# Optimization experiments

Measured on AMD Instinct MI355X. Metric: run time of the kernel, lower is better.

## Reference

```python
import jax, jax.numpy as jnp
import numpy as np

N, OUT, IN = 16384, 2048, 2048

def setup_inputs() -> dict:
    key = jax.random.key(0)
    k1, k2, k3 = jax.random.split(key, 3)
    input_ = jax.random.normal(k1, (N, IN), dtype=jnp.float32)
    # kaiming normal, fan_in mode: std = sqrt(2/fan_in)
    weight = jax.random.normal(k2, (OUT, IN), dtype=jnp.float32) * np.sqrt(2.0 / IN)
    mask = jax.random.randint(k3, (OUT, IN), 0, 2, dtype=jnp.int32)
    return {"input_": input_, "weight": weight, "mask": mask}

def reference(input_, weight, mask):
    # out = x @ (W * mask)^T  -- mask is a fixed binary expander pattern
    masked_w = weight * mask.astype(weight.dtype)  # [OUT, IN]
    return jnp.matmul(input_, masked_w.T)          # [N, OUT]
```

## Files before the change

kernel.cpp:

```cpp
#include <hip/hip_runtime.h>


#define MDIM 16384
#define NDIM 2048
#define KDIM 2048

#define BM 256
#define BN 256
#define NITER (KDIM / 128)
#define GRID_X ((MDIM / BM) * (NDIM / BN))

using f32x4   = __attribute__((ext_vector_type(4))) float;
using bf16x8  = __attribute__((ext_vector_type(8))) __bf16;
using ushort8 = __attribute__((ext_vector_type(8))) unsigned short;

__device__ __forceinline__ unsigned short f2bf(float f) {
  unsigned int u = __builtin_bit_cast(unsigned int, f);
  u = u + 0x7FFFu + ((u >> 16) & 1u);
  return (unsigned short)(u >> 16);
}


__global__ void convert_input_kernel(const float* __restrict__ in,
                                     unsigned short* __restrict__ out) {
  size_t base = ((size_t)blockIdx.x * blockDim.x + threadIdx.x) * 8;
  float4 a = *reinterpret_cast<const float4*>(in + base);
  float4 b = *reinterpret_cast<const float4*>(in + base + 4);
  ushort8 v;
  v[0] = f2bf(a.x); v[1] = f2bf(a.y); v[2] = f2bf(a.z); v[3] = f2bf(a.w);
  v[4] = f2bf(b.x); v[5] = f2bf(b.y); v[6] = f2bf(b.z); v[7] = f2bf(b.w);
  *reinterpret_cast<ushort8*>(out + base) = v;
}

__global__ void convert_weight_kernel(const float* __restrict__ w,
                                      const int* __restrict__ mk,
                                      unsigned short* __restrict__ out) {
  size_t base = ((size_t)blockIdx.x * blockDim.x + threadIdx.x) * 8;
  float4 a = *reinterpret_cast<const float4*>(w + base);
  float4 b = *reinterpret_cast<const float4*>(w + base + 4);
  int4 m0 = *reinterpret_cast<const int4*>(mk + base);
  int4 m1 = *reinterpret_cast<const int4*>(mk + base + 4);
  ushort8 v;
  v[0] = m0.x ? f2bf(a.x) : (unsigned short)0;
  v[1] = m0.y ? f2bf(a.y) : (unsigned short)0;
  v[2] = m0.z ? f2bf(a.z) : (unsigned short)0;
  v[3] = m0.w ? f2bf(a.w) : (unsigned short)0;
  v[4] = m1.x ? f2bf(b.x) : (unsigned short)0;
  v[5] = m1.y ? f2bf(b.y) : (unsigned short)0;
  v[6] = m1.z ? f2bf(b.z) : (unsigned short)0;
  v[7] = m1.w ? f2bf(b.w) : (unsigned short)0;
  *reinterpret_cast<ushort8*>(out + base) = v;
}


__device__ __forceinline__ f32x4 MF(bf16x8 a, bf16x8 b, f32x4 c) {
  return __builtin_amdgcn_mfma_f32_16x16x32_bf16(a, b, c, 0, 0, 0);
}
__device__ __forceinline__ void bar() {
  asm volatile("" ::: "memory");
  __builtin_amdgcn_s_barrier();
  asm volatile("" ::: "memory");
}
#define VMCNT(n) asm volatile("s_waitcnt vmcnt(" #n ")" ::: "memory")

__global__ __launch_bounds__(512, 2) void gemm4p(
    const unsigned short* __restrict__ Abf,
    const unsigned short* __restrict__ Bbf,
    float* __restrict__ C) {
  __shared__ __attribute__((aligned(16))) unsigned short Asl[4 * 8192];
  __shared__ __attribute__((aligned(16))) unsigned short Bsl[4 * 8192];

  int bid = blockIdx.x;
  int wgs = (bid & 7) * (GRID_X / 8) + (bid >> 3);
  int tm = wgs >> 3;
  int tn = wgs & 7;
  int row0 = tm * BM, col0 = tn * BN;

  int t = threadIdx.x;
  int lane = t & 63, wid = t >> 6;
  int wr = wid >> 2, wc = wid & 3;
  int fr = lane & 15, fq = lane >> 4;

  int p0 = (wid * 2 + 0) * 64 + lane;
  int p1 = (wid * 2 + 1) * 64 + lane;
  int r0 = p0 >> 2, kc0 = ((p0 & 3) ^ ((r0 >> 1) & 3)) * 8;
  int r1 = p1 >> 2, kc1 = ((p1 & 3) ^ ((r1 >> 1) & 3)) * 8;
  size_t offA0 = (size_t)(row0 + r0) * KDIM + kc0;
  size_t offA1 = (size_t)(row0 + r1) * KDIM + kc1;
  size_t offB0 = (size_t)(col0 + r0) * KDIM + kc0;
  size_t offB1 = (size_t)(col0 + r1) * KDIM + kc1;
  int ldsw0 = (wid * 2 + 0) * 512;
  int ldsw1 = (wid * 2 + 1) * 512;

  int kxor = (fq ^ ((fr >> 1) & 3)) * 8;
  int aoff = (wr * 128 + fr) * 32 + kxor;
  int boff = (wc * 64 + fr) * 32 + kxor;

  f32x4 acc[8][4];
#pragma unroll
  for (int m = 0; m < 8; ++m)
#pragma unroll
    for (int n = 0; n < 4; ++n) acc[m][n] = f32x4{0.f, 0.f, 0.f, 0.f};

#define SLOT_A(b, kh) (Asl + ((b) * 2 + (kh)) * 8192)
#define SLOT_B(b, kh) (Bsl + ((b) * 2 + (kh)) * 8192)

#define STG(slot, base, o0, o1, ke) do {                                        \
  __builtin_amdgcn_global_load_lds(                                             \
      (const __attribute__((address_space(1))) void*)((base) + (o0) + (ke)),    \
      (__attribute__((address_space(3))) void*)((slot) + ldsw0), 16, 0, 0);     \
  __builtin_amdgcn_global_load_lds(                                             \
      (const __attribute__((address_space(1))) void*)((base) + (o1) + (ke)),    \
      (__attribute__((address_space(3))) void*)((slot) + ldsw1), 16, 0, 0);     \
} while (0)

#define PHASE(b, kh, STAGES, WAITS) do {                                        \
  const unsigned short* _ap = SLOT_A(b, kh) + aoff;                             \
  const unsigned short* _bp = SLOT_B(b, kh) + boff;                             \
  bf16x8 _afr[8], _bfr[4];                                                      \
  _afr[0] = *(const bf16x8*)(_ap);                                              \
  _Pragma("unroll")                                                             \
  for (int _n = 0; _n < 4; ++_n) _bfr[_n] = *(const bf16x8*)(_bp + _n * 512);   \
  _Pragma("unroll")                                                             \
  for (int _m = 1; _m < 8; ++_m) _afr[_m] = *(const bf16x8*)(_ap + _m * 512);   \
  STAGES;                                                                       \
  WAITS;                                                                        \
  bar();                                                                        \
  __builtin_amdgcn_s_setprio(1);                                                \
  _Pragma("unroll")                                                             \
  for (int _m = 0; _m < 8; ++_m)                                                \
    _Pragma("unroll")                                                           \
    for (int _n = 0; _n < 4; ++_n)                                              \
      acc[_m][_n] = MF(_afr[_m], _bfr[_n], acc[_m][_n]);                        \
  __builtin_amdgcn_s_setprio(0);                                                \
  bar();                                                                        \
} while (0)

  STG(SLOT_A(0, 0), Abf, offA0, offA1, 0);
  STG(SLOT_B(0, 0), Bbf, offB0, offB1, 0);
  STG(SLOT_A(0, 1), Abf, offA0, offA1, 32);
  STG(SLOT_B(0, 1), Bbf, offB0, offB1, 32);
  STG(SLOT_A(1, 0), Abf, offA0, offA1, 64);
  STG(SLOT_B(1, 0), Bbf, offB0, offB1, 64);
  VMCNT(8);
  bar();

  for (int i = 0; i < NITER - 1; ++i) {
    int kb = i * 128;
    PHASE(0, 0, { STG(SLOT_A(1, 1), Abf, offA0, offA1, kb + 96);
                  STG(SLOT_B(1, 1), Bbf, offB0, offB1, kb + 96); }, VMCNT(8));
    PHASE(0, 1, { STG(SLOT_A(0, 0), Abf, offA0, offA1, kb + 128);
                  STG(SLOT_B(0, 0), Bbf, offB0, offB1, kb + 128); }, VMCNT(8));
    PHASE(1, 0, { STG(SLOT_A(0, 1), Abf, offA0, offA1, kb + 160);
                  STG(SLOT_B(0, 1), Bbf, offB0, offB1, kb + 160); }, VMCNT(8));
    PHASE(1, 1, { STG(SLOT_A(1, 0), Abf, offA0, offA1, kb + 192);
                  STG(SLOT_B(1, 0), Bbf, offB0, offB1, kb + 192); }, VMCNT(8));
  }
  {
    int kb = (NITER - 1) * 128;
    PHASE(0, 0, { STG(SLOT_A(1, 1), Abf, offA0, offA1, kb + 96);
                  STG(SLOT_B(1, 1), Bbf, offB0, offB1, kb + 96); }, VMCNT(8));
    PHASE(0, 1, , VMCNT(4));
    PHASE(1, 0, , VMCNT(0));
    PHASE(1, 1, , );
  }

  size_t crow = (size_t)(row0 + wr * 128 + fq * 4);
  int ccol = col0 + wc * 64 + fr;
#pragma unroll
  for (int m = 0; m < 8; ++m)
#pragma unroll
    for (int n = 0; n < 4; ++n) {
      float* cp = C + (crow + m * 16) * NDIM + ccol + n * 16;
#pragma unroll
      for (int e = 0; e < 4; ++e) cp[(size_t)e * NDIM] = acc[m][n][e];
    }
#undef PHASE
#undef STG
#undef SLOT_A
#undef SLOT_B
}


__global__ __launch_bounds__(256) void gemm_fused_fallback(
    const float* __restrict__ Afp,
    const float* __restrict__ Wfp,
    const int* __restrict__ Mk,
    float* __restrict__ C) {
  __shared__ unsigned short As[128 * 32];
  __shared__ unsigned short Bs[128 * 32];
  int bid = blockIdx.x;
  int nwg = (MDIM / 128) * (NDIM / 128);
  int wg = (bid & 7) * (nwg / 8) + (bid >> 3);
  int tm = wg >> 4, tn = wg & 15;
  int row0 = tm * 128, col0 = tn * 128;
  int t = threadIdx.x;
  int lane = t & 63, wv = t >> 6;
  int wr = wv >> 1, wc = wv & 1;
  int fr = lane & 15, fq = lane >> 4;
  f32x4 acc[4][4];
#pragma unroll
  for (int i = 0; i < 4; ++i)
#pragma unroll
    for (int j = 0; j < 4; ++j) acc[i][j] = f32x4{0.f, 0.f, 0.f, 0.f};
  for (int kt = 0; kt < KDIM; kt += 32) {
#pragma unroll
    for (int j = 0; j < 2; ++j) {
      int c = j * 256 + t;
      int r = c >> 2;
      int ko = (c & 3) * 8;
      const float* ga = Afp + (size_t)(row0 + r) * KDIM + kt + ko;
      float4 a0 = *reinterpret_cast<const float4*>(ga);
      float4 a1 = *reinterpret_cast<const float4*>(ga + 4);
      ushort8 va;
      va[0] = f2bf(a0.x); va[1] = f2bf(a0.y); va[2] = f2bf(a0.z); va[3] = f2bf(a0.w);
      va[4] = f2bf(a1.x); va[5] = f2bf(a1.y); va[6] = f2bf(a1.z); va[7] = f2bf(a1.w);
      *reinterpret_cast<ushort8*>(As + (size_t)c * 8) = va;
      const float* gw = Wfp + (size_t)(col0 + r) * KDIM + kt + ko;
      const int* gm = Mk + (size_t)(col0 + r) * KDIM + kt + ko;
      float4 w0 = *reinterpret_cast<const float4*>(gw);
      float4 w1 = *reinterpret_cast<const float4*>(gw + 4);
      int4 m0 = *reinterpret_cast<const int4*>(gm);
      int4 m1 = *reinterpret_cast<const int4*>(gm + 4);
      ushort8 vb;
      vb[0] = m0.x ? f2bf(w0.x) : (unsigned short)0;
      vb[1] = m0.y ? f2bf(w0.y) : (unsigned short)0;
      vb[2] = m0.z ? f2bf(w0.z) : (unsigned short)0;
      vb[3] = m0.w ? f2bf(w0.w) : (unsigned short)0;
      vb[4] = m1.x ? f2bf(w1.x) : (unsigned short)0;
      vb[5] = m1.y ? f2bf(w1.y) : (unsigned short)0;
      vb[6] = m1.z ? f2bf(w1.z) : (unsigned short)0;
      vb[7] = m1.w ? f2bf(w1.w) : (unsigned short)0;
      *reinterpret_cast<ushort8*>(Bs + (size_t)c * 8) = vb;
    }
    __syncthreads();
    bf16x8 af[4], bfr[4];
#pragma unroll
    for (int m2 = 0; m2 < 4; ++m2)
      af[m2] = *reinterpret_cast<const bf16x8*>(As + (wr * 64 + m2 * 16 + fr) * 32 + fq * 8);
#pragma unroll
    for (int n2 = 0; n2 < 4; ++n2)
      bfr[n2] = *reinterpret_cast<const bf16x8*>(Bs + (wc * 64 + n2 * 16 + fr) * 32 + fq * 8);
#pragma unroll
    for (int m2 = 0; m2 < 4; ++m2)
#pragma unroll
      for (int n2 = 0; n2 < 4; ++n2)
        acc[m2][n2] = MF(af[m2], bfr[n2], acc[m2][n2]);
    __syncthreads();
  }
#pragma unroll
  for (int m2 = 0; m2 < 4; ++m2)
#pragma unroll
    for (int n2 = 0; n2 < 4; ++n2) {
      size_t r0 = (size_t)(row0 + wr * 64 + m2 * 16 + fq * 4);
      size_t c0 = (size_t)(col0 + wc * 64 + n2 * 16 + fr);
#pragma unroll
      for (int i = 0; i < 4; ++i) C[(r0 + i) * NDIM + c0] = acc[m2][n2][i];
    }
}


extern "C" void kernel_launch(void* const* d_in, const int* in_sizes, int n_in,
                              void* d_out, int out_size, void* d_ws, size_t ws_size,
                              hipStream_t stream) {
  const float* input  = (const float*)d_in[0];
  const float* weight = (const float*)d_in[1];
  const int*   mask   = (const int*)d_in[2];
  float* out = (float*)d_out;

  const size_t needA = (size_t)MDIM * KDIM * sizeof(unsigned short);
  const size_t needB = (size_t)NDIM * KDIM * sizeof(unsigned short);

  if (ws_size >= needA + needB) {
    unsigned short* Abf = (unsigned short*)d_ws;
    unsigned short* Bbf = (unsigned short*)((char*)d_ws + needA);
    convert_input_kernel<<<(MDIM * (size_t)KDIM / 8) / 256, 256, 0, stream>>>(input, Abf);
    convert_weight_kernel<<<(NDIM * (size_t)KDIM / 8) / 256, 256, 0, stream>>>(weight, mask, Bbf);
    gemm4p<<<GRID_X, 512, 0, stream>>>(Abf, Bbf, out);
  } else {
    int nwg = (MDIM / 128) * (NDIM / 128);
    gemm_fused_fallback<<<nwg, 256, 0, stream>>>(input, weight, mask, out);
  }
}
```

Measured before the change: 182.4 us.

## Software-pipeline LDS fragment reads by prefetching next phase during MFMAs

Restructures the main loop so that LDS-to-register reads for the next K sub-slice are issued inside the current phase's MFMA loop. A-fragments are reloaded row by row after use, and B-fragments are double-buffered in two register sets. This hides LDS read latency behind matrix math instead of stalling before each MFMA block. It also simplifies the second staging address to a fixed offset from the first. The cost is higher register pressure from the extra B buffer and a rotated phase order with a prologue and epilogue, which risks spills under the 512x2 launch bounds.

```diff
diff --git a/kernel.cpp b/kernel.cpp
--- a/kernel.cpp
+++ b/kernel.cpp
@@ -7,7 +7,6 @@
 
 #define BM 256
 #define BN 256
-#define NITER (KDIM / 128)
 #define GRID_X ((MDIM / BM) * (NDIM / BN))
 
 using f32x4   = __attribute__((ext_vector_type(4))) float;
@@ -63,7 +62,7 @@
 }
 #define VMCNT(n) asm volatile("s_waitcnt vmcnt(" #n ")" ::: "memory")
 
-__global__ __launch_bounds__(512, 2) void gemm4p(
+__global__ __launch_bounds__(512, 2) void gemm_pl(
     const unsigned short* __restrict__ Abf,
     const unsigned short* __restrict__ Bbf,
     float* __restrict__ C) {
@@ -82,15 +81,10 @@
   int fr = lane & 15, fq = lane >> 4;
 
   int p0 = (wid * 2 + 0) * 64 + lane;
-  int p1 = (wid * 2 + 1) * 64 + lane;
   int r0 = p0 >> 2, kc0 = ((p0 & 3) ^ ((r0 >> 1) & 3)) * 8;
-  int r1 = p1 >> 2, kc1 = ((p1 & 3) ^ ((r1 >> 1) & 3)) * 8;
   size_t offA0 = (size_t)(row0 + r0) * KDIM + kc0;
-  size_t offA1 = (size_t)(row0 + r1) * KDIM + kc1;
   size_t offB0 = (size_t)(col0 + r0) * KDIM + kc0;
-  size_t offB1 = (size_t)(col0 + r1) * KDIM + kc1;
   int ldsw0 = (wid * 2 + 0) * 512;
-  int ldsw1 = (wid * 2 + 1) * 512;
 
   int kxor = (fq ^ ((fr >> 1) & 3)) * 8;
   int aoff = (wr * 128 + fr) * 32 + kxor;
@@ -102,67 +96,81 @@
 #pragma unroll
     for (int n = 0; n < 4; ++n) acc[m][n] = f32x4{0.f, 0.f, 0.f, 0.f};
 
+  bf16x8 afr[8], bfrA[4], bfrB[4];
+
 #define SLOT_A(b, kh) (Asl + ((b) * 2 + (kh)) * 8192)
 #define SLOT_B(b, kh) (Bsl + ((b) * 2 + (kh)) * 8192)
 
-#define STG(slot, base, o0, o1, ke) do {                                        \
+#define STG(slot, base, o0, ke) do {                                            \
   __builtin_amdgcn_global_load_lds(                                             \
       (const __attribute__((address_space(1))) void*)((base) + (o0) + (ke)),    \
       (__attribute__((address_space(3))) void*)((slot) + ldsw0), 16, 0, 0);     \
   __builtin_amdgcn_global_load_lds(                                             \
-      (const __attribute__((address_space(1))) void*)((base) + (o1) + (ke)),    \
-      (__attribute__((address_space(3))) void*)((slot) + ldsw1), 16, 0, 0);     \
+      (const __attribute__((address_space(1))) void*)((base) + (o0) + 32768 +   \
+                                                      (ke)),                    \
+      (__attribute__((address_space(3))) void*)((slot) + ldsw0 + 512), 16, 0,   \
+      0);                                                                       \
 } while (0)
 
-#define PHASE(b, kh, STAGES, WAITS) do {                                        \
-  const unsigned short* _ap = SLOT_A(b, kh) + aoff;                             \
-  const unsigned short* _bp = SLOT_B(b, kh) + boff;                             \
-  bf16x8 _afr[8], _bfr[4];                                                      \
-  _afr[0] = *(const bf16x8*)(_ap);                                              \
-  _Pragma("unroll")                                                             \
-  for (int _n = 0; _n < 4; ++_n) _bfr[_n] = *(const bf16x8*)(_bp + _n * 512);   \
-  _Pragma("unroll")                                                             \
-  for (int _m = 1; _m < 8; ++_m) _afr[_m] = *(const bf16x8*)(_ap + _m * 512);   \
+#define PHASE(rb, rkh, SETR, SETU, STAGES, WAITS) do {                          \
   STAGES;                                                                       \
   WAITS;                                                                        \
   bar();                                                                        \
+  const unsigned short* _rpa = SLOT_A(rb, rkh) + aoff;                          \
+  const unsigned short* _rpb = SLOT_B(rb, rkh) + boff;                          \
+  _Pragma("unroll")                                                             \
+  for (int _n = 0; _n < 4; ++_n)                                                \
+    SETR[_n] = *(const bf16x8*)(_rpb + _n * 512);                               \
   __builtin_amdgcn_s_setprio(1);                                                \
   _Pragma("unroll")                                                             \
-  for (int _m = 0; _m < 8; ++_m)                                                \
+  for (int _m = 0; _m < 8; ++_m) {                                              \
     _Pragma("unroll")                                                           \
     for (int _n = 0; _n < 4; ++_n)                                              \
-      acc[_m][_n] = MF(_afr[_m], _bfr[_n], acc[_m][_n]);                        \
+      acc[_m][_n] = MF(afr[_m], SETU[_n], acc[_m][_n]);                         \
+    afr[_m] = *(const bf16x8*)(_rpa + _m * 512);                                \
+  }                                                                             \
   __builtin_amdgcn_s_setprio(0);                                                \
   bar();                                                                        \
 } while (0)
 
-  STG(SLOT_A(0, 0), Abf, offA0, offA1, 0);
-  STG(SLOT_B(0, 0), Bbf, offB0, offB1, 0);
-  STG(SLOT_A(0, 1), Abf, offA0, offA1, 32);
-  STG(SLOT_B(0, 1), Bbf, offB0, offB1, 32);
-  STG(SLOT_A(1, 0), Abf, offA0, offA1, 64);
-  STG(SLOT_B(1, 0), Bbf, offB0, offB1, 64);
+  STG(SLOT_A(0, 0), Abf, offA0, 0);
+  STG(SLOT_B(0, 0), Bbf, offB0, 0);
+  STG(SLOT_A(0, 1), Abf, offA0, 32);
+  STG(SLOT_B(0, 1), Bbf, offB0, 32);
+  STG(SLOT_A(1, 0), Abf, offA0, 64);
+  STG(SLOT_B(1, 0), Bbf, offB0, 64);
   VMCNT(8);
   bar();
-
-  for (int i = 0; i < NITER - 1; ++i) {
+  {
+    const unsigned short* pa = SLOT_A(0, 0) + aoff;
+    const unsigned short* pb = SLOT_B(0, 0) + boff;
+#pragma unroll
+    for (int m = 0; m < 8; ++m) afr[m] = *(const bf16x8*)(pa + m * 512);
+#pragma unroll
+    for (int n = 0; n < 4; ++n) bfrA[n] = *(const bf16x8*)(pb + n * 512);
+  }
+
+  for (int i = 0; i < 15; ++i) {
     int kb = i * 128;
-    PHASE(0, 0, { STG(SLOT_A(1, 1), Abf, offA0, offA1, kb + 96);
-                  STG(SLOT_B(1, 1), Bbf, offB0, offB1, kb + 96); }, VMCNT(8));
-    PHASE(0, 1, { STG(SLOT_A(0, 0), Abf, offA0, offA1, kb + 128);
-                  STG(SLOT_B(0, 0), Bbf, offB0, offB1, kb + 128); }, VMCNT(8));
-    PHASE(1, 0, { STG(SLOT_A(0, 1), Abf, offA0, offA1, kb + 160);
-                  STG(SLOT_B(0, 1), Bbf, offB0, offB1, kb + 160); }, VMCNT(8));
-    PHASE(1, 1, { STG(SLOT_A(1, 0), Abf, offA0, offA1, kb + 192);
-                  STG(SLOT_B(1, 0), Bbf, offB0, offB1, kb + 192); }, VMCNT(8));
-  }
+    PHASE(0, 1, bfrB, bfrA, { STG(SLOT_A(1, 1), Abf, offA0, kb + 96);
+                              STG(SLOT_B(1, 1), Bbf, offB0, kb + 96); }, VMCNT(8));
+    PHASE(1, 0, bfrA, bfrB, { STG(SLOT_A(0, 0), Abf, offA0, kb + 128);
+                              STG(SLOT_B(0, 0), Bbf, offB0, kb + 128); }, VMCNT(8));
+    PHASE(1, 1, bfrB, bfrA, { STG(SLOT_A(0, 1), Abf, offA0, kb + 160);
+                              STG(SLOT_B(0, 1), Bbf, offB0, kb + 160); }, VMCNT(8));
+    PHASE(0, 0, bfrA, bfrB, { STG(SLOT_A(1, 0), Abf, offA0, kb + 192);
+                              STG(SLOT_B(1, 0), Bbf, offB0, kb + 192); }, VMCNT(8));
+  }
+  PHASE(0, 1, bfrB, bfrA, { STG(SLOT_A(1, 1), Abf, offA0, 2016);
+                            STG(SLOT_B(1, 1), Bbf, offB0, 2016); }, VMCNT(8));
+  PHASE(1, 0, bfrA, bfrB, , VMCNT(4));
+  PHASE(1, 1, bfrB, bfrA, , VMCNT(0));
   {
-    int kb = (NITER - 1) * 128;
-    PHASE(0, 0, { STG(SLOT_A(1, 1), Abf, offA0, offA1, kb + 96);
-                  STG(SLOT_B(1, 1), Bbf, offB0, offB1, kb + 96); }, VMCNT(8));
-    PHASE(0, 1, , VMCNT(4));
-    PHASE(1, 0, , VMCNT(0));
-    PHASE(1, 1, , );
+#pragma unroll
+    for (int m = 0; m < 8; ++m)
+#pragma unroll
+      for (int n = 0; n < 4; ++n)
+        acc[m][n] = MF(afr[m], bfrB[n], acc[m][n]);
   }
 
   size_t crow = (size_t)(row0 + wr * 128 + fq * 4);
@@ -276,7 +284,7 @@
     unsigned short* Bbf = (unsigned short*)((char*)d_ws + needA);
     convert_input_kernel<<<(MDIM * (size_t)KDIM / 8) / 256, 256, 0, stream>>>(input, Abf);
     convert_weight_kernel<<<(NDIM * (size_t)KDIM / 8) / 256, 256, 0, stream>>>(weight, mask, Bbf);
-    gemm4p<<<GRID_X, 512, 0, stream>>>(Abf, Bbf, out);
+    gemm_pl<<<GRID_X, 512, 0, stream>>>(Abf, Bbf, out);
   } else {
     int nwg = (MDIM / 128) * (NDIM / 128);
     gemm_fused_fallback<<<nwg, 256, 0, stream>>>(input, weight, mask, out);
```

Result: slower. 187.4 us (+2.7%).

## Shrink GEMM tile to 256x128 with skewed A/B staging for higher occupancy

Applied to the files above, without the earlier changes.

Replaces the 256x256 four-phase GEMM with a 256x128 tile kernel (launch bounds 512 threads, 4 blocks per CU). Each wave now holds a 64x64 accumulator. LDS holds a three-slot ring for A and a two-slot ring for B, and the B prefetch runs one 32-wide K step behind the A prefetch. The aim is more resident waves for latency hiding and less LDS and register use per block. The cost is more global and LDS traffic per FLOP, since each A tile is reused across only 128 columns, and a barrier on every 32-wide K step.

```diff
diff --git a/kernel.cpp b/kernel.cpp
--- a/kernel.cpp
+++ b/kernel.cpp
@@ -6,8 +6,7 @@
 #define KDIM 2048
 
 #define BM 256
-#define BN 256
-#define NITER (KDIM / 128)
+#define BN 128
 #define GRID_X ((MDIM / BM) * (NDIM / BN))
 
 using f32x4   = __attribute__((ext_vector_type(4))) float;
@@ -63,122 +62,115 @@
 }
 #define VMCNT(n) asm volatile("s_waitcnt vmcnt(" #n ")" ::: "memory")
 
-__global__ __launch_bounds__(512, 2) void gemm4p(
+__global__ __launch_bounds__(512, 4) void gemm_tlp(
     const unsigned short* __restrict__ Abf,
     const unsigned short* __restrict__ Bbf,
     float* __restrict__ C) {
-  __shared__ __attribute__((aligned(16))) unsigned short Asl[4 * 8192];
-  __shared__ __attribute__((aligned(16))) unsigned short Bsl[4 * 8192];
+  __shared__ __attribute__((aligned(16))) unsigned short Asl[3 * 8192];
+  __shared__ __attribute__((aligned(16))) unsigned short Bsl[2 * 4096];
 
   int bid = blockIdx.x;
   int wgs = (bid & 7) * (GRID_X / 8) + (bid >> 3);
-  int tm = wgs >> 3;
-  int tn = wgs & 7;
+  int tm = wgs >> 4;
+  int tn = wgs & 15;
   int row0 = tm * BM, col0 = tn * BN;
 
   int t = threadIdx.x;
   int lane = t & 63, wid = t >> 6;
-  int wr = wid >> 2, wc = wid & 3;
+  int wr = wid >> 1, wc = wid & 1;
   int fr = lane & 15, fq = lane >> 4;
 
-  int p0 = (wid * 2 + 0) * 64 + lane;
-  int p1 = (wid * 2 + 1) * 64 + lane;
-  int r0 = p0 >> 2, kc0 = ((p0 & 3) ^ ((r0 >> 1) & 3)) * 8;
-  int r1 = p1 >> 2, kc1 = ((p1 & 3) ^ ((r1 >> 1) & 3)) * 8;
-  size_t offA0 = (size_t)(row0 + r0) * KDIM + kc0;
-  size_t offA1 = (size_t)(row0 + r1) * KDIM + kc1;
-  size_t offB0 = (size_t)(col0 + r0) * KDIM + kc0;
-  size_t offB1 = (size_t)(col0 + r1) * KDIM + kc1;
-  int ldsw0 = (wid * 2 + 0) * 512;
-  int ldsw1 = (wid * 2 + 1) * 512;
+  int p0 = (wid * 2) * 64 + lane;
+  int ra0 = p0 >> 2, ka0 = ((p0 & 3) ^ ((ra0 >> 1) & 3)) * 8;
+  int p1 = p0 + 64;
+  int ra1 = p1 >> 2, ka1 = ((p1 & 3) ^ ((ra1 >> 1) & 3)) * 8;
+  size_t offA0 = (size_t)(row0 + ra0) * KDIM + ka0;
+  size_t offA1 = (size_t)(row0 + ra1) * KDIM + ka1;
+  int ldswA0 = (wid * 2) * 512, ldswA1 = (wid * 2 + 1) * 512;
+  int q = wid * 64 + lane;
+  int rb = q >> 2, kb_ = ((q & 3) ^ ((rb >> 1) & 3)) * 8;
+  size_t offB0 = (size_t)(col0 + rb) * KDIM + kb_;
+  int ldswB = wid * 512;
 
   int kxor = (fq ^ ((fr >> 1) & 3)) * 8;
-  int aoff = (wr * 128 + fr) * 32 + kxor;
+  int aoff = (wr * 64 + fr) * 32 + kxor;
   int boff = (wc * 64 + fr) * 32 + kxor;
 
-  f32x4 acc[8][4];
-#pragma unroll
-  for (int m = 0; m < 8; ++m)
+  f32x4 acc[4][4];
+#pragma unroll
+  for (int m = 0; m < 4; ++m)
 #pragma unroll
     for (int n = 0; n < 4; ++n) acc[m][n] = f32x4{0.f, 0.f, 0.f, 0.f};
 
-#define SLOT_A(b, kh) (Asl + ((b) * 2 + (kh)) * 8192)
-#define SLOT_B(b, kh) (Bsl + ((b) * 2 + (kh)) * 8192)
-
-#define STG(slot, base, o0, o1, ke) do {                                        \
+#define STGA(sa, ke) do {                                                       \
   __builtin_amdgcn_global_load_lds(                                             \
-      (const __attribute__((address_space(1))) void*)((base) + (o0) + (ke)),    \
-      (__attribute__((address_space(3))) void*)((slot) + ldsw0), 16, 0, 0);     \
+      (const __attribute__((address_space(1))) void*)(Abf + offA0 + (ke)),      \
+      (__attribute__((address_space(3))) void*)(Asl + (sa) * 8192 + ldswA0),    \
+      16, 0, 0);                                                                \
   __builtin_amdgcn_global_load_lds(                                             \
-      (const __attribute__((address_space(1))) void*)((base) + (o1) + (ke)),    \
-      (__attribute__((address_space(3))) void*)((slot) + ldsw1), 16, 0, 0);     \
+      (const __attribute__((address_space(1))) void*)(Abf + offA1 + (ke)),      \
+      (__attribute__((address_space(3))) void*)(Asl + (sa) * 8192 + ldswA1),    \
+      16, 0, 0);                                                                \
 } while (0)
-
-#define PHASE(b, kh, STAGES, WAITS) do {                                        \
-  const unsigned short* _ap = SLOT_A(b, kh) + aoff;                             \
-  const unsigned short* _bp = SLOT_B(b, kh) + boff;                             \
-  bf16x8 _afr[8], _bfr[4];                                                      \
-  _afr[0] = *(const bf16x8*)(_ap);                                              \
-  _Pragma("unroll")                                                             \
-  for (int _n = 0; _n < 4; ++_n) _bfr[_n] = *(const bf16x8*)(_bp + _n * 512);   \
-  _Pragma("unroll")                                                             \
-  for (int _m = 1; _m < 8; ++_m) _afr[_m] = *(const bf16x8*)(_ap + _m * 512);   \
+#define STGB(sb, ke) do {                                                       \
+  __builtin_amdgcn_global_load_lds(                                             \
+      (const __attribute__((address_space(1))) void*)(Bbf + offB0 + (ke)),      \
+      (__attribute__((address_space(3))) void*)(Bsl + (sb) * 4096 + ldswB),     \
+      16, 0, 0);                                                                \
+} while (0)
+
+#define PH(sa, sb, STAGES, WAITS) do {                                          \
   STAGES;                                                                       \
   WAITS;                                                                        \
   bar();                                                                        \
+  const unsigned short* _ap = Asl + (sa) * 8192 + aoff;                         \
+  const unsigned short* _bp = Bsl + (sb) * 4096 + boff;                         \
+  bf16x8 _af[4], _bf[4];                                                        \
+  _Pragma("unroll")                                                             \
+  for (int _m = 0; _m < 4; ++_m) _af[_m] = *(const bf16x8*)(_ap + _m * 512);    \
+  _Pragma("unroll")                                                             \
+  for (int _n = 0; _n < 4; ++_n) _bf[_n] = *(const bf16x8*)(_bp + _n * 512);    \
   __builtin_amdgcn_s_setprio(1);                                                \
   _Pragma("unroll")                                                             \
-  for (int _m = 0; _m < 8; ++_m)                                                \
+  for (int _m = 0; _m < 4; ++_m)                                                \
     _Pragma("unroll")                                                           \
     for (int _n = 0; _n < 4; ++_n)                                              \
-      acc[_m][_n] = MF(_afr[_m], _bfr[_n], acc[_m][_n]);                        \
+      acc[_m][_n] = MF(_af[_m], _bf[_n], acc[_m][_n]);                          \
   __builtin_amdgcn_s_setprio(0);                                                \
   bar();                                                                        \
 } while (0)
 
-  STG(SLOT_A(0, 0), Abf, offA0, offA1, 0);
-  STG(SLOT_B(0, 0), Bbf, offB0, offB1, 0);
-  STG(SLOT_A(0, 1), Abf, offA0, offA1, 32);
-  STG(SLOT_B(0, 1), Bbf, offB0, offB1, 32);
-  STG(SLOT_A(1, 0), Abf, offA0, offA1, 64);
-  STG(SLOT_B(1, 0), Bbf, offB0, offB1, 64);
-  VMCNT(8);
-  bar();
-
-  for (int i = 0; i < NITER - 1; ++i) {
-    int kb = i * 128;
-    PHASE(0, 0, { STG(SLOT_A(1, 1), Abf, offA0, offA1, kb + 96);
-                  STG(SLOT_B(1, 1), Bbf, offB0, offB1, kb + 96); }, VMCNT(8));
-    PHASE(0, 1, { STG(SLOT_A(0, 0), Abf, offA0, offA1, kb + 128);
-                  STG(SLOT_B(0, 0), Bbf, offB0, offB1, kb + 128); }, VMCNT(8));
-    PHASE(1, 0, { STG(SLOT_A(0, 1), Abf, offA0, offA1, kb + 160);
-                  STG(SLOT_B(0, 1), Bbf, offB0, offB1, kb + 160); }, VMCNT(8));
-    PHASE(1, 1, { STG(SLOT_A(1, 0), Abf, offA0, offA1, kb + 192);
-                  STG(SLOT_B(1, 0), Bbf, offB0, offB1, kb + 192); }, VMCNT(8));
+  STGA(0, 0);
+  STGA(1, 32);
+  STGB(0, 0);
+
+  for (int i = 0; i < 10; ++i) {
+    int kb = i * 192;
+    PH(0, 0, { STGA(2, kb + 64);  STGB(1, kb + 32);  }, VMCNT(3));
+    PH(1, 1, { STGA(0, kb + 96);  STGB(0, kb + 64);  }, VMCNT(3));
+    PH(2, 0, { STGA(1, kb + 128); STGB(1, kb + 96);  }, VMCNT(3));
+    PH(0, 1, { STGA(2, kb + 160); STGB(0, kb + 128); }, VMCNT(3));
+    PH(1, 0, { STGA(0, kb + 192); STGB(1, kb + 160); }, VMCNT(3));
+    PH(2, 1, { STGA(1, kb + 224); STGB(0, kb + 192); }, VMCNT(3));
   }
-  {
-    int kb = (NITER - 1) * 128;
-    PHASE(0, 0, { STG(SLOT_A(1, 1), Abf, offA0, offA1, kb + 96);
-                  STG(SLOT_B(1, 1), Bbf, offB0, offB1, kb + 96); }, VMCNT(8));
-    PHASE(0, 1, , VMCNT(4));
-    PHASE(1, 0, , VMCNT(0));
-    PHASE(1, 1, , );
-  }
-
-  size_t crow = (size_t)(row0 + wr * 128 + fq * 4);
+  PH(0, 0, { STGA(2, 1984); STGB(1, 1952); }, VMCNT(3));
+  PH(1, 1, { STGA(0, 2016); STGB(0, 1984); }, VMCNT(3));
+  PH(2, 0, { STGB(1, 2016); }, VMCNT(1));
+  PH(0, 1, , VMCNT(0));
+
+  size_t crow = (size_t)(row0 + wr * 64 + fq * 4);
   int ccol = col0 + wc * 64 + fr;
 #pragma unroll
-  for (int m = 0; m < 8; ++m)
+  for (int m = 0; m < 4; ++m)
 #pragma unroll
     for (int n = 0; n < 4; ++n) {
       float* cp = C + (crow + m * 16) * NDIM + ccol + n * 16;
 #pragma unroll
       for (int e = 0; e < 4; ++e) cp[(size_t)e * NDIM] = acc[m][n][e];
     }
-#undef PHASE
-#undef STG
-#undef SLOT_A
-#undef SLOT_B
+#undef PH
+#undef STGA
+#undef STGB
 }
 
 
@@ -276,7 +268,7 @@
     unsigned short* Bbf = (unsigned short*)((char*)d_ws + needA);
     convert_input_kernel<<<(MDIM * (size_t)KDIM / 8) / 256, 256, 0, stream>>>(input, Abf);
     convert_weight_kernel<<<(NDIM * (size_t)KDIM / 8) / 256, 256, 0, stream>>>(weight, mask, Bbf);
-    gemm4p<<<GRID_X, 512, 0, stream>>>(Abf, Bbf, out);
+    gemm_tlp<<<GRID_X, 512, 0, stream>>>(Abf, Bbf, out);
   } else {
     int nwg = (MDIM / 128) * (NDIM / 128);
     gemm_fused_fallback<<<nwg, 256, 0, stream>>>(input, weight, mask, out);
```

Result: slower. 187.3 us (+2.7%).
